# Performance work log

Measured on AMD Instinct MI355X. Metric: run time of the kernel, lower is better.

## Reference

```python
import jax, jax.numpy as jnp
import numpy as np

NB_KNN = (10, 20, 100, 200)
MAX_K = 200
T = 0.07
NUM_CLASSES = 1000


def setup_inputs() -> dict:
    key = jax.random.key(0)
    k1, k2, k3 = jax.random.split(key, 3)
    features_rank = jax.random.normal(k1, (512, 1024), dtype=jnp.float32)
    train_features = jax.random.normal(k2, (100000, 1024), dtype=jnp.float32)
    train_labels = jax.random.randint(k3, (100000,), 0, NUM_CLASSES, dtype=jnp.int64 if jax.config.jax_enable_x64 else jnp.int32)
    return {"features_rank": features_rank, "train_features": train_features, "train_labels": train_labels}


def reference(features_rank, train_features, train_labels):
    # similarity: [B, N] = [B, d] @ [d, N]  (train_features_rank_T in torch)
    sims = features_rank @ train_features.T
    # top-max_k neighbors, sorted descending (matches torch.topk(largest=True, sorted=True))
    topk_sims, indices = jax.lax.top_k(sims, MAX_K)          # [B, max_k]
    neighbors_labels = train_labels[indices]                 # gather: [B, max_k]
    # temperature softmax over the max_k neighbor similarities
    weights = jax.nn.softmax(topk_sims / T, axis=1)          # [B, max_k]
    B = features_rank.shape[0]
    rows = jnp.arange(B)[:, None]                            # [B, 1] broadcast row index
    def probas_for_k(k):
        # fused scatter-add replaces one_hot(labels) * weights -> sum over k
        return jnp.zeros((B, NUM_CLASSES), weights.dtype).at[rows, neighbors_labels[:, :k]].add(weights[:, :k])
    # stacked along axis 0 in nb_knn order: [len(nb_knn), B, num_classes]
    return jnp.stack([probas_for_k(k) for k in NB_KNN])
```

## Files before the change

kernel.cpp:

```cpp
#include <hip/hip_runtime.h>
#include <float.h>
#include <math.h>

#define NROWS 512
#define DIM 1024
#define NTRAIN 100000
#define MAXK 200
#define NCLS 1000
#define CAPF 128
#define INV_T (1.0f/0.07f)
#define NKS (DIM/32)
#define NTILE 784
#define NPAD (NTILE*128)
#define FMARGIN 5.0f

typedef short s16x8 __attribute__((ext_vector_type(8)));
typedef unsigned short u16x8 __attribute__((ext_vector_type(8)));
typedef unsigned int u32x4 __attribute__((ext_vector_type(4)));
typedef float f32x4 __attribute__((ext_vector_type(4)));

__device__ __forceinline__ void gl_lds16(const void* g, void* l) {
    __builtin_amdgcn_global_load_lds(
        (const __attribute__((address_space(1))) unsigned int*)g,
        (__attribute__((address_space(3))) unsigned int*)l, 16, 0, 0);
}
__device__ __forceinline__ unsigned short f2bf(float x) {
    unsigned u = __float_as_uint(x);
    return (unsigned short)((u + 0x7FFFu + ((u >> 16) & 1u)) >> 16);
}
__device__ __forceinline__ float bf2f(unsigned short b) {
    return __uint_as_float(((unsigned)b) << 16);
}

__global__ __launch_bounds__(256) void convert_bf16(
    const float* __restrict__ in, unsigned short* __restrict__ out, long long n)
{
    long long i0 = ((long long)blockIdx.x * 256 + threadIdx.x) * 8;
    long long stride = (long long)gridDim.x * 2048;
    for (long long i = i0; i < n; i += stride) {
        float4 v0 = *reinterpret_cast<const float4*>(&in[i]);
        float4 v1 = *reinterpret_cast<const float4*>(&in[i + 4]);
        u16x8 o;
        o[0] = f2bf(v0.x); o[1] = f2bf(v0.y); o[2] = f2bf(v0.z); o[3] = f2bf(v0.w);
        o[4] = f2bf(v1.x); o[5] = f2bf(v1.y); o[6] = f2bf(v1.z); o[7] = f2bf(v1.w);
        *reinterpret_cast<u16x8*>(&out[i]) = o;
    }
}

__global__ __launch_bounds__(256) void gemm_fused(
    const unsigned short* __restrict__ Ab, const float* __restrict__ B,
    unsigned short* __restrict__ simsb)
{
    __shared__ __align__(16) char sm[3][24576];
    const int tid = threadIdx.x;
    const int lane = tid & 63;
    const int wave = tid >> 6;

    const int nwg = gridDim.x;
    const int wg = (blockIdx.x & 7) * (nwg >> 3) + (blockIdx.x >> 3);
    const int mt = wg & 3, nt = wg >> 2;
    const int m0 = mt * 128, n0 = nt * 128;
    const int wm = wave >> 1, wn = wave & 1;

    size_t gA[2];
    #pragma unroll
    for (int i = 0; i < 2; ++i) {
        int c = wave * 64 + i * 256 + lane;
        int rr = c >> 2, q = c & 3;
        int slot = q ^ ((rr >> 1) & 3);
        gA[i] = (size_t)(m0 + rr) * DIM + slot * 8;
    }
    const int ldsA0 = (wave * 64) * 16;
    const int ldsA1 = (wave * 64 + 256) * 16;

    size_t gB[4];
    #pragma unroll
    for (int i = 0; i < 4; ++i) {
        int c = wave * 256 + i * 64 + lane;
        int rr = c >> 3, q = c & 7;
        int slot = q ^ (rr & 7);
        int brow = n0 + rr;
        if (brow > NTRAIN - 1) brow = NTRAIN - 1;
        gB[i] = (size_t)brow * DIM + slot * 4;
    }
    const int ldsB[4] = { 8192 + (wave * 256) * 16, 8192 + (wave * 256 + 64) * 16,
                          8192 + (wave * 256 + 128) * 16, 8192 + (wave * 256 + 192) * 16 };

    f32x4 acc[4][4] = {};

    auto stage = [&](int b, int k0) {
        char* base = &sm[b][0];
        gl_lds16(Ab + gA[0] + k0, base + ldsA0);
        gl_lds16(Ab + gA[1] + k0, base + ldsA1);
        #pragma unroll
        for (int i = 0; i < 4; ++i)
            gl_lds16(B + gB[i] + k0, base + ldsB[i]);
    };

    const int qq = lane >> 4;
    const int r16 = lane & 15;

    stage(0, 0);
    stage(1, 32);

    for (int t = 0; t < NKS; ++t) {
        if (t + 1 < NKS) {
            asm volatile("s_waitcnt vmcnt(6)" ::: "memory");
        } else {
            asm volatile("s_waitcnt vmcnt(0)" ::: "memory");
        }
        __builtin_amdgcn_s_barrier();
        __builtin_amdgcn_sched_barrier(0);

        if (t + 2 < NKS) stage((t + 2) % 3, (t + 2) * 32);

        const char* sa = &sm[t % 3][0];
        const char* sbB = &sm[t % 3][8192];

        s16x8 bv[4];
        #pragma unroll
        for (int n = 0; n < 4; ++n) {
            int rr = wn * 64 + n * 16 + r16;
            const char* rowb = sbB + (rr * 8) * 16;
            int c0 = (2 * qq) ^ (rr & 7);
            int c1 = (2 * qq + 1) ^ (rr & 7);
            u32x4 fa = *reinterpret_cast<const u32x4*>(rowb + c0 * 16);
            u32x4 fb = *reinterpret_cast<const u32x4*>(rowb + c1 * 16);
            unsigned w0 = __builtin_amdgcn_perm(fa[1], fa[0], 0x07060302u);
            unsigned w1 = __builtin_amdgcn_perm(fa[3], fa[2], 0x07060302u);
            unsigned w2 = __builtin_amdgcn_perm(fb[1], fb[0], 0x07060302u);
            unsigned w3 = __builtin_amdgcn_perm(fb[3], fb[2], 0x07060302u);
            u32x4 packed = { w0, w1, w2, w3 };
            bv[n] = __builtin_bit_cast(s16x8, packed);
        }
        #pragma unroll
        for (int m = 0; m < 4; ++m) {
            int rr = wm * 64 + m * 16 + r16;
            int cch = rr * 4 + (qq ^ ((rr >> 1) & 3));
            s16x8 av = *reinterpret_cast<const s16x8*>(sa + cch * 16);
            #pragma unroll
            for (int n = 0; n < 4; ++n)
                acc[m][n] = __builtin_amdgcn_mfma_f32_16x16x32_bf16(av, bv[n], acc[m][n], 0, 0, 0);
        }
    }

    const int q4 = (lane >> 4) * 4;
    const int cL = lane & 15;
    #pragma unroll
    for (int m = 0; m < 4; ++m)
        #pragma unroll
        for (int j = 0; j < 4; ++j) {
            int orow = m0 + wm * 64 + m * 16 + q4 + j;
            unsigned short* dst = simsb + (size_t)orow * NPAD + n0 + wn * 64 + cL;
            #pragma unroll
            for (int n = 0; n < 4; ++n)
                dst[n * 16] = f2bf(acc[m][n][j]);
        }
}

__global__ __launch_bounds__(512) void maxfilter(
    const unsigned short* __restrict__ simsb, int* __restrict__ ci, int* __restrict__ cc)
{
    __shared__ float wmax[8];
    __shared__ float s_max;
    __shared__ int s_cnt;
    const int tid = threadIdx.x;
    const int r = blockIdx.x;
    const unsigned short* srow = simsb + (size_t)r * NPAD;

    float m = -FLT_MAX;
    for (int i = tid * 8; i < NTRAIN; i += 4096) {
        u16x8 v = *reinterpret_cast<const u16x8*>(&srow[i]);
        #pragma unroll
        for (int j = 0; j < 8; ++j) m = fmaxf(m, bf2f(v[j]));
    }
    #pragma unroll
    for (int s = 32; s >= 1; s >>= 1) m = fmaxf(m, __shfl_xor(m, s));
    if ((tid & 63) == 0) wmax[tid >> 6] = m;
    if (tid == 0) s_cnt = 0;
    __syncthreads();
    if (tid == 0) {
        float mm = wmax[0];
        #pragma unroll
        for (int w = 1; w < 8; ++w) mm = fmaxf(mm, wmax[w]);
        s_max = mm;
    }
    __syncthreads();
    const float Lv = s_max - FMARGIN;

    for (int i = tid * 8; i < NTRAIN; i += 4096) {
        u16x8 v = *reinterpret_cast<const u16x8*>(&srow[i]);
        #pragma unroll
        for (int j = 0; j < 8; ++j) {
            if (bf2f(v[j]) >= Lv) {
                int p = atomicAdd(&s_cnt, 1);
                if (p < CAPF) ci[(size_t)r * CAPF + p] = i + j;
            }
        }
    }
    __syncthreads();
    if (tid == 0) cc[r] = min(s_cnt, CAPF);
}

__global__ __launch_bounds__(256) void exact_refine(
    const float* __restrict__ A, const float* __restrict__ B,
    const int* __restrict__ ci, const int* __restrict__ cc, float* __restrict__ ev)
{
    __shared__ float sa[DIM];
    const int tid = threadIdx.x;
    const int r = blockIdx.x;
    *reinterpret_cast<float4*>(&sa[tid * 4]) =
        *reinterpret_cast<const float4*>(&A[(size_t)r * DIM + tid * 4]);
    __syncthreads();
    const int lane = tid & 63;
    const int wave = tid >> 6;
    const int M = min(cc[r], CAPF);

    for (int i = wave; i < M; i += 4) {
        int idx = ci[(size_t)r * CAPF + i];
        const float* brow = B + (size_t)idx * DIM;
        float s = 0.f;
        #pragma unroll
        for (int j = 0; j < 4; ++j) {
            float4 bvv = *reinterpret_cast<const float4*>(&brow[j * 256 + lane * 4]);
            float4 avv = *reinterpret_cast<const float4*>(&sa[j * 256 + lane * 4]);
            s = fmaf(avv.x, bvv.x, s);
            s = fmaf(avv.y, bvv.y, s);
            s = fmaf(avv.z, bvv.z, s);
            s = fmaf(avv.w, bvv.w, s);
        }
        #pragma unroll
        for (int m2 = 32; m2 >= 1; m2 >>= 1) s += __shfl_xor(s, m2);
        if (lane == 0) ev[(size_t)r * CAPF + i] = s;
    }
}

__global__ __launch_bounds__(256) void finalize_small(
    const float* __restrict__ ev, const int* __restrict__ ci, const int* __restrict__ cc,
    const int* __restrict__ labels, float* __restrict__ out)
{
    __shared__ float sval[CAPF];
    __shared__ int   sidx[CAPF];
    __shared__ float cls[NCLS];
    __shared__ float s_sum;
    const int tid = threadIdx.x;
    const int r = blockIdx.x;
    const int M = min(cc[r], CAPF);

    for (int i = tid; i < CAPF; i += 256) {
        if (i < M) { sval[i] = ev[(size_t)r * CAPF + i]; sidx[i] = ci[(size_t)r * CAPF + i]; }
        else { sval[i] = -FLT_MAX; sidx[i] = 0x7FFFFFFF; }
    }
    __syncthreads();

    for (int k = 2; k <= CAPF; k <<= 1)
        for (int j = k >> 1; j > 0; j >>= 1) {
            for (int i = tid; i < CAPF; i += 256) {
                int l = i ^ j;
                if (l > i) {
                    float av = sval[i], bv2 = sval[l];
                    int ai = sidx[i], bi = sidx[l];
                    bool iGTl = (av > bv2) || (av == bv2 && ai < bi);
                    bool sw = ((i & k) == 0) ? (!iGTl) : iGTl;
                    if (sw) { sval[i] = bv2; sval[l] = av; sidx[i] = bi; sidx[l] = ai; }
                }
            }
            __syncthreads();
        }

    float mx = sval[0];
    if (tid == 0) s_sum = 0.f;
    __syncthreads();
    float part = 0.f;
    for (int i = tid; i < M; i += 256) {
        float e = expf((sval[i] - mx) * INV_T);
        sval[i] = e;
        part += e;
    }
    atomicAdd(&s_sum, part);
    __syncthreads();
    float inv = 1.f / s_sum;
    for (int i = tid; i < M; i += 256) {
        sval[i] *= inv;
        sidx[i] = labels[sidx[i]];
    }
    for (int c = tid; c < NCLS; c += 256) cls[c] = 0.f;
    __syncthreads();

    const int KS[4] = {10, 20, 100, 200};
    int prev = 0;
    for (int s = 0; s < 4; ++s) {
        int hi = min(KS[s], M);
        for (int i = prev + tid; i < hi; i += 256)
            atomicAdd(&cls[sidx[i]], sval[i]);
        __syncthreads();
        float* o = out + ((size_t)s * NROWS + r) * NCLS;
        for (int c = tid; c < NCLS; c += 256) o[c] = cls[c];
        __syncthreads();
        prev = hi;
    }
}

extern "C" void kernel_launch(void* const* d_in, const int* in_sizes, int n_in,
                              void* d_out, int out_size, void* d_ws, size_t ws_size,
                              hipStream_t stream)
{
    const float* A = (const float*)d_in[0];
    const float* B = (const float*)d_in[1];
    const int* labels = (const int*)d_in[2];
    float* out = (float*)d_out;

    char* ws = (char*)d_ws;
    size_t off = 0;
    auto carve = [&](size_t bytes) -> void* {
        void* p = ws + off;
        off = (off + bytes + 255) & ~(size_t)255;
        return p;
    };
    unsigned short* Ab = (unsigned short*)carve((size_t)NROWS * DIM * 2);
    int*   ci = (int*)carve((size_t)NROWS * CAPF * 4);
    float* ev = (float*)carve((size_t)NROWS * CAPF * 4);
    int*   cc = (int*)carve((size_t)NROWS * 4);
    unsigned short* simsb = (unsigned short*)carve((size_t)NROWS * NPAD * 2);

    convert_bf16<<<128, 256, 0, stream>>>(A, Ab, (long long)NROWS * DIM);

    gemm_fused<<<4 * NTILE, 256, 0, stream>>>(Ab, B, simsb);

    maxfilter<<<NROWS, 512, 0, stream>>>(simsb, ci, cc);

    exact_refine<<<NROWS, 256, 0, stream>>>(A, B, ci, cc, ev);

    finalize_small<<<NROWS, 256, 0, stream>>>(ev, ci, cc, labels, out);
}
```

Measured before the change: 270.7 us.

## Convert B tile to bf16 in registers before LDS store, shrinking LDS staging

Train-feature fp32 tiles are no longer copied straight into LDS with global_load_lds. Each thread now loads them into registers three steps ahead, packs them to bf16 with perm, and writes a swizzled bf16 tile into LDS. This halves LDS footprint and read traffic for B and drops the per-step perm work in the MMA loop. In exchange it adds register pressure from three staging buffers, explicit VMEM and LDS wait management, and LDS writes that pass through VGPRs.

```diff
diff --git a/kernel.cpp b/kernel.cpp
--- a/kernel.cpp
+++ b/kernel.cpp
@@ -51,7 +51,7 @@
     const unsigned short* __restrict__ Ab, const float* __restrict__ B,
     unsigned short* __restrict__ simsb)
 {
-    __shared__ __align__(16) char sm[3][24576];
+    __shared__ __align__(16) unsigned short sm[3][8192];
     const int tid = threadIdx.x;
     const int lane = tid & 63;
     const int wave = tid >> 6;
@@ -73,76 +73,104 @@
     const int ldsA0 = (wave * 64) * 16;
     const int ldsA1 = (wave * 64 + 256) * 16;
 
-    size_t gB[4];
-    #pragma unroll
-    for (int i = 0; i < 4; ++i) {
-        int c = wave * 256 + i * 64 + lane;
-        int rr = c >> 3, q = c & 7;
-        int slot = q ^ (rr & 7);
-        int brow = n0 + rr;
-        if (brow > NTRAIN - 1) brow = NTRAIN - 1;
-        gB[i] = (size_t)brow * DIM + slot * 4;
-    }
-    const int ldsB[4] = { 8192 + (wave * 256) * 16, 8192 + (wave * 256 + 64) * 16,
-                          8192 + (wave * 256 + 128) * 16, 8192 + (wave * 256 + 192) * 16 };
+    const int rr0 = tid >> 2, q0 = tid & 3;
+    const int rr1 = rr0 + 64;
+    int brow0 = n0 + rr0; if (brow0 > NTRAIN - 1) brow0 = NTRAIN - 1;
+    int brow1 = n0 + rr1; if (brow1 > NTRAIN - 1) brow1 = NTRAIN - 1;
+    const size_t gb0 = (size_t)brow0 * DIM + q0 * 8;
+    const size_t gb1 = (size_t)brow1 * DIM + q0 * 8;
+    const int lo0 = 8192 + (rr0 * 4 + (q0 ^ ((rr0 >> 1) & 3))) * 16;
+    const int lo1 = 8192 + (rr1 * 4 + (q0 ^ ((rr1 >> 1) & 3))) * 16;
 
     f32x4 acc[4][4] = {};
-
-    auto stage = [&](int b, int k0) {
-        char* base = &sm[b][0];
+    u32x4 S0[2][2], S1[2][2], S2[2][2];
+
+    auto stageA = [&](int b, int k0) {
+        char* base = (char*)&sm[b][0];
         gl_lds16(Ab + gA[0] + k0, base + ldsA0);
         gl_lds16(Ab + gA[1] + k0, base + ldsA1);
-        #pragma unroll
-        for (int i = 0; i < 4; ++i)
-            gl_lds16(B + gB[i] + k0, base + ldsB[i]);
     };
+
+#define LOADB(S, K0)                                                           \
+    {                                                                          \
+        S[0][0] = *reinterpret_cast<const u32x4*>(B + gb0 + (K0));             \
+        S[0][1] = *reinterpret_cast<const u32x4*>(B + gb0 + (K0) + 4);         \
+        S[1][0] = *reinterpret_cast<const u32x4*>(B + gb1 + (K0));             \
+        S[1][1] = *reinterpret_cast<const u32x4*>(B + gb1 + (K0) + 4);         \
+    }
+#define WRITEB(BI, S)                                                          \
+    {                                                                          \
+        char* dstB = (char*)&sm[BI][0];                                        \
+        u32x4 p0 = { __builtin_amdgcn_perm(S[0][0][1], S[0][0][0], 0x07060302u), \
+                     __builtin_amdgcn_perm(S[0][0][3], S[0][0][2], 0x07060302u), \
+                     __builtin_amdgcn_perm(S[0][1][1], S[0][1][0], 0x07060302u), \
+                     __builtin_amdgcn_perm(S[0][1][3], S[0][1][2], 0x07060302u) }; \
+        *reinterpret_cast<u32x4*>(dstB + lo0) = p0;                            \
+        u32x4 p1 = { __builtin_amdgcn_perm(S[1][0][1], S[1][0][0], 0x07060302u), \
+                     __builtin_amdgcn_perm(S[1][0][3], S[1][0][2], 0x07060302u), \
+                     __builtin_amdgcn_perm(S[1][1][1], S[1][1][0], 0x07060302u), \
+                     __builtin_amdgcn_perm(S[1][1][3], S[1][1][2], 0x07060302u) }; \
+        *reinterpret_cast<u32x4*>(dstB + lo1) = p1;                            \
+    }
 
     const int qq = lane >> 4;
     const int r16 = lane & 15;
 
-    stage(0, 0);
-    stage(1, 32);
-
-    for (int t = 0; t < NKS; ++t) {
-        if (t + 1 < NKS) {
-            asm volatile("s_waitcnt vmcnt(6)" ::: "memory");
-        } else {
-            asm volatile("s_waitcnt vmcnt(0)" ::: "memory");
-        }
-        __builtin_amdgcn_s_barrier();
-        __builtin_amdgcn_sched_barrier(0);
-
-        if (t + 2 < NKS) stage((t + 2) % 3, (t + 2) * 32);
-
-        const char* sa = &sm[t % 3][0];
-        const char* sbB = &sm[t % 3][8192];
-
-        s16x8 bv[4];
-        #pragma unroll
-        for (int n = 0; n < 4; ++n) {
-            int rr = wn * 64 + n * 16 + r16;
-            const char* rowb = sbB + (rr * 8) * 16;
-            int c0 = (2 * qq) ^ (rr & 7);
-            int c1 = (2 * qq + 1) ^ (rr & 7);
-            u32x4 fa = *reinterpret_cast<const u32x4*>(rowb + c0 * 16);
-            u32x4 fb = *reinterpret_cast<const u32x4*>(rowb + c1 * 16);
-            unsigned w0 = __builtin_amdgcn_perm(fa[1], fa[0], 0x07060302u);
-            unsigned w1 = __builtin_amdgcn_perm(fa[3], fa[2], 0x07060302u);
-            unsigned w2 = __builtin_amdgcn_perm(fb[1], fb[0], 0x07060302u);
-            unsigned w3 = __builtin_amdgcn_perm(fb[3], fb[2], 0x07060302u);
-            u32x4 packed = { w0, w1, w2, w3 };
-            bv[n] = __builtin_bit_cast(s16x8, packed);
-        }
-        #pragma unroll
-        for (int m = 0; m < 4; ++m) {
-            int rr = wm * 64 + m * 16 + r16;
-            int cch = rr * 4 + (qq ^ ((rr >> 1) & 3));
-            s16x8 av = *reinterpret_cast<const s16x8*>(sa + cch * 16);
-            #pragma unroll
-            for (int n = 0; n < 4; ++n)
-                acc[m][n] = __builtin_amdgcn_mfma_f32_16x16x32_bf16(av, bv[n], acc[m][n], 0, 0, 0);
-        }
-    }
+    LOADB(S0, 0)
+    stageA(0, 0);
+    LOADB(S1, 32)
+    stageA(1, 32);
+    LOADB(S2, 64)
+    asm volatile("s_waitcnt vmcnt(12)" ::: "memory");
+    __builtin_amdgcn_sched_barrier(0);
+    WRITEB(0, S0)
+    asm volatile("s_waitcnt lgkmcnt(0)" ::: "memory");
+
+#define STEP(T, SW, SL)                                                        \
+    {                                                                          \
+        if ((T) + 2 < NKS) {                                                   \
+            asm volatile("s_waitcnt vmcnt(6)" ::: "memory");                   \
+        } else if ((T) + 1 < NKS) {                                            \
+            asm volatile("s_waitcnt vmcnt(2)" ::: "memory");                   \
+        } else {                                                               \
+            asm volatile("s_waitcnt vmcnt(0)" ::: "memory");                   \
+        }                                                                      \
+        __builtin_amdgcn_s_barrier();                                          \
+        __builtin_amdgcn_sched_barrier(0);                                     \
+        if ((T) + 1 < NKS) WRITEB(((T) + 1) % 3, SW)                           \
+        if ((T) + 2 < NKS) stageA(((T) + 2) % 3, ((T) + 2) * 32);              \
+        if ((T) + 3 < NKS) LOADB(SL, ((T) + 3) * 32)                           \
+        const unsigned short* sa = &sm[(T) % 3][0];                            \
+        const unsigned short* sb = &sm[(T) % 3][4096];                         \
+        s16x8 bv[4];                                                           \
+        _Pragma("unroll")                                                      \
+        for (int n = 0; n < 4; ++n) {                                          \
+            int rr = wn * 64 + n * 16 + r16;                                   \
+            int cch = rr * 4 + (qq ^ ((rr >> 1) & 3));                         \
+            bv[n] = *reinterpret_cast<const s16x8*>(&sb[cch * 8]);             \
+        }                                                                      \
+        _Pragma("unroll")                                                      \
+        for (int m = 0; m < 4; ++m) {                                          \
+            int rr = wm * 64 + m * 16 + r16;                                   \
+            int cch = rr * 4 + (qq ^ ((rr >> 1) & 3));                         \
+            s16x8 av = *reinterpret_cast<const s16x8*>(&sa[cch * 8]);          \
+            _Pragma("unroll")                                                  \
+            for (int n = 0; n < 4; ++n)                                        \
+                acc[m][n] = __builtin_amdgcn_mfma_f32_16x16x32_bf16(av, bv[n], acc[m][n], 0, 0, 0); \
+        }                                                                      \
+        asm volatile("s_waitcnt lgkmcnt(0)" ::: "memory");                     \
+    }
+
+    for (int tt = 0; tt < 30; tt += 3) {
+        STEP(tt,     S1, S0)
+        STEP(tt + 1, S2, S1)
+        STEP(tt + 2, S0, S2)
+    }
+    STEP(30, S1, S0)
+    STEP(31, S2, S1)
+#undef STEP
+#undef LOADB
+#undef WRITEB
 
     const int q4 = (lane >> 4) * 4;
     const int cL = lane & 15;
```

Result: no change. 275.8 us (+1.9%).
